# Kernel optimization log

Measured on AMD Instinct MI355X. Metric: run time of the kernel, lower is better.

## Reference

```python
import jax, jax.numpy as jnp
import numpy as np

B, T, D = 2, 2048, 1024
H, HD = 16, 64  # num_heads, key_size

def setup_inputs() -> dict:
    key = jax.random.key(0)
    ks = jax.random.split(key, 5)
    s = 1.0 / np.sqrt(D)  # VarianceScaling(1.0, fan_in) approx
    return {
        "query": jax.random.normal(ks[0], (B, T, D), dtype=jnp.float32),
        "wq": jax.random.normal(ks[1], (D, H * HD), dtype=jnp.float32) * s,
        "bq": jnp.zeros((H * HD,), dtype=jnp.float32),
        "wk": jax.random.normal(ks[2], (D, H * HD), dtype=jnp.float32) * s,
        "bk": jnp.zeros((H * HD,), dtype=jnp.float32),
        "wv": jax.random.normal(ks[3], (D, H * HD), dtype=jnp.float32) * s,
        "bv": jnp.zeros((H * HD,), dtype=jnp.float32),
        "wo": jax.random.normal(ks[4], (H * HD, D), dtype=jnp.float32) * (1.0 / np.sqrt(H * HD)),
        "bo": jnp.zeros((D,), dtype=jnp.float32),
    }

def reference(query, wq, bq, wk, bk, wv, bv, wo, bo):
    b, t, _ = query.shape
    proj = lambda w, bias: (query @ w + bias).reshape(b, t, H, HD)
    q = proj(wq, bq) / np.sqrt(HD).astype(np.float32)  # fixed scaling on queries
    k = proj(wk, bk)
    v = proj(wv, bv)
    logits = jnp.einsum('bthd,bThd->bhtT', q, k)  # [B,H,T,T]
    causal = jnp.tril(jnp.ones((t, t), dtype=logits.dtype))
    logits = logits - 1e10 * (1.0 - causal)
    weights = jax.nn.softmax(logits, axis=-1)
    attn = jnp.einsum('bhtT,bThd->bthd', weights, v)
    attn_vec = attn.reshape(b, t, H * HD)
    return attn_vec @ wo + bo
```

## Files before the change

kernel.cpp:

```cpp
#include <hip/hip_runtime.h>
#include <hip/hip_bf16.h>
#include <stdint.h>
#include <math.h>

typedef short bf16x8 __attribute__((ext_vector_type(8)));
typedef float f32x4 __attribute__((ext_vector_type(4)));
typedef unsigned u32x4v __attribute__((ext_vector_type(4)));
typedef __hip_bfloat16 bf16;

#define MFMA16(a, b, c) __builtin_amdgcn_mfma_f32_16x16x32_bf16((a), (b), (c), 0, 0, 0)

__device__ __forceinline__ void glds16(const void* g, void* l) {
  __builtin_amdgcn_global_load_lds((const __attribute__((address_space(1))) void*)g,
                                   (__attribute__((address_space(3))) void*)l, 16, 0, 0);
}

__device__ __forceinline__ bf16x8 ld8(const bf16* p) {
  return *reinterpret_cast<const bf16x8*>(p);
}

__device__ __forceinline__ void pl32swap(unsigned& a, unsigned& b) {
  asm volatile("v_permlane32_swap_b32 %0, %1" : "+v"(a), "+v"(b));
}
__device__ __forceinline__ void pl16swap(unsigned& a, unsigned& b) {
  asm volatile("v_permlane16_swap_b32 %0, %1" : "+v"(a), "+v"(b));
}


__global__ void k_prep(const float* __restrict__ query,
                       const float* __restrict__ wq, const float* __restrict__ wk,
                       const float* __restrict__ wv, const float* __restrict__ wo,
                       bf16* __restrict__ X, bf16* __restrict__ Wqkvt, bf16* __restrict__ Wot) {
  __shared__ float tile[32][33];
  const int z = blockIdx.z;
  if (z < 4) {
    const float* src = (z == 0) ? wq : (z == 1) ? wk : (z == 2) ? wv : wo;
    bf16* dst = (z < 3) ? (Wqkvt + (size_t)z * 1024 * 1024) : Wot;
    const int tx = threadIdx.x & 31, ty = threadIdx.x >> 5;
    const int x = blockIdx.x * 32 + tx;
    const int y0 = blockIdx.y * 32;
#pragma unroll
    for (int i = 0; i < 4; ++i) tile[ty + i * 8][tx] = src[(size_t)(y0 + ty + i * 8) * 1024 + x];
    __syncthreads();
#pragma unroll
    for (int i = 0; i < 4; ++i) {
      int c = blockIdx.x * 32 + ty + i * 8;
      dst[(size_t)c * 1024 + y0 + tx] = __float2bfloat16(tile[tx][ty + i * 8]);
    }
  } else {
    const int vb = (z - 4) * 1024 + blockIdx.y * 32 + blockIdx.x;
    const int i = vb * 256 + threadIdx.x;
    float4 v = reinterpret_cast<const float4*>(query)[i];
    bf16 a0 = __float2bfloat16(v.x), a1 = __float2bfloat16(v.y);
    bf16 a2 = __float2bfloat16(v.z), a3 = __float2bfloat16(v.w);
    ushort4 r;
    r.x = reinterpret_cast<unsigned short&>(a0);
    r.y = reinterpret_cast<unsigned short&>(a1);
    r.z = reinterpret_cast<unsigned short&>(a2);
    r.w = reinterpret_cast<unsigned short&>(a3);
    reinterpret_cast<ushort4*>(X)[i] = r;
  }
}


__device__ __forceinline__ void gemm_core(const bf16* __restrict__ A, const bf16* __restrict__ Bt,
                                          int K, int arow0, int bcol0,
                                          bf16* As, bf16* Bs, f32x4 acc[4][4]) {
  const int tid = threadIdx.x, lane = tid & 63, w = tid >> 6;
  const int rsub = lane >> 3, slot = lane & 7;
  const int srcslot = slot ^ rsub;
  const int wrow = (w >> 1) * 64, wcol = (w & 1) * 64;
  const int lr = lane & 15, lg = lane >> 4;
  const int nkt = K >> 6;
  for (int kt = 0; kt < nkt; ++kt) {
    const int k0 = kt * 64;
    if (kt) __syncthreads();
#pragma unroll
    for (int i = 0; i < 4; ++i) {
      const int chunk = w * 4 + i;
      glds16(A + (size_t)(arow0 + chunk * 8 + rsub) * K + k0 + srcslot * 8, As + chunk * 512);
      glds16(Bt + (size_t)(bcol0 + chunk * 8 + rsub) * K + k0 + srcslot * 8, Bs + chunk * 512);
    }
    __syncthreads();
#pragma unroll
    for (int kk = 0; kk < 2; ++kk) {
      bf16x8 af[4], bfv[4];
#pragma unroll
      for (int m = 0; m < 4; ++m) {
        const int row = wrow + m * 16 + lr;
        const int byte = (row * 128 + ((kk * 32 + lg * 8) << 1)) ^ ((row & 7) << 4);
        af[m] = *reinterpret_cast<const bf16x8*>(reinterpret_cast<const char*>(As) + byte);
      }
#pragma unroll
      for (int n = 0; n < 4; ++n) {
        const int row = wcol + n * 16 + lr;
        const int byte = (row * 128 + ((kk * 32 + lg * 8) << 1)) ^ ((row & 7) << 4);
        bfv[n] = *reinterpret_cast<const bf16x8*>(reinterpret_cast<const char*>(Bs) + byte);
      }
#pragma unroll
      for (int m = 0; m < 4; ++m)
#pragma unroll
        for (int n = 0; n < 4; ++n) acc[m][n] = MFMA16(af[m], bfv[n], acc[m][n]);
    }
  }
}


__global__ __launch_bounds__(256) void k_gemm_qkv(
    const bf16* __restrict__ X, const bf16* __restrict__ Wt,
    const float* __restrict__ bq, const float* __restrict__ bk, const float* __restrict__ bv,
    bf16* __restrict__ Qo, bf16* __restrict__ Ko, bf16* __restrict__ Vt) {
  __shared__ bf16 As[128 * 64], Bs[128 * 64];
  f32x4 acc[4][4];
#pragma unroll
  for (int i = 0; i < 4; ++i)
#pragma unroll
    for (int j = 0; j < 4; ++j) acc[i][j] = (f32x4){0.f, 0.f, 0.f, 0.f};
  const int arow0 = blockIdx.y * 128, bcol0 = blockIdx.x * 128;
  gemm_core(X, Wt, 1024, arow0, bcol0, As, Bs, acc);
  const int lane = threadIdx.x & 63, w = threadIdx.x >> 6;
  const int wrow = (w >> 1) * 64, wcol = (w & 1) * 64;
  const int lr = lane & 15, lg = lane >> 4;
  const float QSCALE = 0.125f * 1.4426950408889634f;
#pragma unroll
  for (int mi = 0; mi < 4; ++mi) {
#pragma unroll
    for (int ni = 0; ni < 4; ++ni) {
      const int r0 = arow0 + wrow + mi * 16 + lg * 4;
      const int col = bcol0 + wcol + ni * 16 + lr;
      const int which = col >> 10, cw = col & 1023, h = cw >> 6, hd = cw & 63;
      const int b = r0 >> 11, t0 = r0 & 2047;
      if (which == 2) {
        const float bias = bv[cw];
        ushort4 pk;
#pragma unroll
        for (int j = 0; j < 4; ++j) {
          bf16 hv = __float2bfloat16(acc[mi][ni][j] + bias);
          reinterpret_cast<unsigned short*>(&pk)[j] = reinterpret_cast<unsigned short&>(hv);
        }
        *reinterpret_cast<ushort4*>(Vt + ((size_t)((b * 16 + h) * 64 + hd)) * 2048 + t0) = pk;
      } else {
        const float bias = which ? bk[cw] : bq[cw];
        const float scale = which ? 1.0f : QSCALE;
        bf16* dst = which ? Ko : Qo;
#pragma unroll
        for (int j = 0; j < 4; ++j) {
          float v = (acc[mi][ni][j] + bias) * scale;
          dst[((size_t)((b * 16 + h) * 2048) + t0 + j) * 64 + hd] = __float2bfloat16(v);
        }
      }
    }
  }
}


__global__ __launch_bounds__(256) void k_attn(const bf16* __restrict__ Q, const bf16* __restrict__ Kc,
                                              const bf16* __restrict__ Vt, bf16* __restrict__ attn) {
  __shared__ bf16 Ks[2][64 * 64];
  __shared__ bf16 Vs[2][64 * 64];
  const int lane = threadIdx.x & 63, w = threadIdx.x >> 6;
  const int lr = lane & 15, lg = lane >> 4;
  const int rsub = lane >> 3, slot = lane & 7;
  const int srcslot = slot ^ rsub;
  const int bh = blockIdx.x;
  const int qt = 31 - blockIdx.y;
  const int b = bh >> 4, h = bh & 15;
  const bf16* Qp = Q + (size_t)bh * 2048 * 64;
  const bf16* Kp = Kc + (size_t)bh * 2048 * 64;
  const bf16* Vp = Vt + (size_t)bh * 64 * 2048;

  const int q0 = qt * 64 + w * 16;
  const bf16x8 qa0 = ld8(Qp + (size_t)(q0 + lr) * 64 + lg * 8);
  const bf16x8 qa1 = ld8(Qp + (size_t)(q0 + lr) * 64 + 32 + lg * 8);
  f32x4 o[4], ol;
#pragma unroll
  for (int n = 0; n < 4; ++n) o[n] = (f32x4){0.f, 0.f, 0.f, 0.f};
  ol = (f32x4){0.f, 0.f, 0.f, 0.f};
  const int nkv = qt + 1;
  const float MBIAS = -8.0f * 1.4426950408889634f;
  const f32x4 minit = {MBIAS, MBIAS, MBIAS, MBIAS};
  const short one_bf = (short)0x3F80;
  const bf16x8 ones = {one_bf, one_bf, one_bf, one_bf, one_bf, one_bf, one_bf, one_bf};

#pragma unroll
  for (int i = 0; i < 2; ++i) {
    const int ck = w * 2 + i;
    glds16(Kp + (size_t)(ck * 8 + rsub) * 64 + srcslot * 8, &Ks[0][ck * 512]);
    glds16(Vp + (size_t)(ck * 8 + rsub) * 2048 + srcslot * 8, &Vs[0][ck * 512]);
  }
  __syncthreads();
  int cur = 0;

#pragma unroll 1
  for (int it = 0; it < nkv; ++it) {
    if (it + 1 < nkv) {
#pragma unroll
      for (int i = 0; i < 2; ++i) {
        const int ck = w * 2 + i;
        glds16(Kp + (size_t)((it + 1) * 64 + ck * 8 + rsub) * 64 + srcslot * 8, &Ks[cur ^ 1][ck * 512]);
        glds16(Vp + (size_t)(ck * 8 + rsub) * 2048 + (it + 1) * 64 + srcslot * 8, &Vs[cur ^ 1][ck * 512]);
      }
    }
    f32x4 s[4];
    const char* Kb = reinterpret_cast<const char*>(&Ks[cur][0]);
#pragma unroll
    for (int n = 0; n < 4; ++n) {
      const int row = n * 16 + lr;
      const int rsw = (row & 7) << 4;
      bf16x8 kb0 = *reinterpret_cast<const bf16x8*>(Kb + ((row * 128 + lg * 16) ^ rsw));
      bf16x8 kb1 = *reinterpret_cast<const bf16x8*>(Kb + ((row * 128 + 64 + lg * 16) ^ rsw));
      s[n] = MFMA16(kb0, qa0, minit);
      s[n] = MFMA16(kb1, qa1, s[n]);
    }
    if (it == nkv - 1) {
      const int qme = q0 + lr - it * 64 - lg * 4;
#pragma unroll
      for (int n = 0; n < 4; ++n)
#pragma unroll
        for (int j = 0; j < 4; ++j)
          if (n * 16 + j > qme) s[n][j] = -1e30f;
    }
    float p[4][4];
#pragma unroll
    for (int n = 0; n < 4; ++n)
#pragma unroll
      for (int j = 0; j < 4; ++j) p[n][j] = __builtin_amdgcn_exp2f(s[n][j]);
    unsigned pw[4][2];
#pragma unroll
    for (int n = 0; n < 4; ++n) {
      pw[n][0] = __builtin_amdgcn_perm(__float_as_uint(p[n][1]), __float_as_uint(p[n][0]), 0x07060302u);
      pw[n][1] = __builtin_amdgcn_perm(__float_as_uint(p[n][3]), __float_as_uint(p[n][2]), 0x07060302u);
    }
#pragma unroll
    for (int n1 = 0; n1 < 2; ++n1)
#pragma unroll
      for (int hh = 0; hh < 2; ++hh) {
        pl32swap(pw[2 * n1][hh], pw[2 * n1 + 1][hh]);
        pl16swap(pw[2 * n1][hh], pw[2 * n1 + 1][hh]);
      }
    bf16x8 pa[2];
#pragma unroll
    for (int n1 = 0; n1 < 2; ++n1) {
      u32x4v tv = (u32x4v){pw[2 * n1][0], pw[2 * n1][1], pw[2 * n1 + 1][0], pw[2 * n1 + 1][1]};
      pa[n1] = __builtin_bit_cast(bf16x8, tv);
    }
    ol = MFMA16(pa[0], ones, ol);
    ol = MFMA16(pa[1], ones, ol);
    const char* Vb = reinterpret_cast<const char*>(&Vs[cur][0]);
#pragma unroll
    for (int n2 = 0; n2 < 4; ++n2) {
#pragma unroll
      for (int kc = 0; kc < 2; ++kc) {
        const int row = n2 * 16 + lr;
        const int rsw = (row & 7) << 4;
        bf16x8 vb = *reinterpret_cast<const bf16x8*>(Vb + ((row * 128 + (kc * 32 + lg * 8) * 2) ^ rsw));
        o[n2] = MFMA16(pa[kc], vb, o[n2]);
      }
    }
    __syncthreads();
    cur ^= 1;
  }
#pragma unroll
  for (int j = 0; j < 4; ++j) {
    const float inv = 1.0f / ol[j];
    const int qq = q0 + lg * 4 + j;
#pragma unroll
    for (int n2 = 0; n2 < 4; ++n2)
      attn[((size_t)(b * 2048 + qq)) * 1024 + h * 64 + n2 * 16 + lr] = __float2bfloat16(o[n2][j] * inv);
  }
}


__global__ __launch_bounds__(256) void k_gemm_out(const bf16* __restrict__ A, const bf16* __restrict__ Wot,
                                                  const float* __restrict__ bo, float* __restrict__ out) {
  __shared__ bf16 As[64 * 64], Bs[128 * 64];
  f32x4 acc[4][2];
#pragma unroll
  for (int i = 0; i < 4; ++i)
#pragma unroll
    for (int j = 0; j < 2; ++j) acc[i][j] = (f32x4){0.f, 0.f, 0.f, 0.f};
  const int arow0 = blockIdx.y * 64, bcol0 = blockIdx.x * 128;
  const int lane = threadIdx.x & 63, w = threadIdx.x >> 6;
  const int rsub = lane >> 3, slot = lane & 7;
  const int srcslot = slot ^ rsub;
  const int lr = lane & 15, lg = lane >> 4;
  for (int kt = 0; kt < 16; ++kt) {
    const int k0 = kt * 64;
    if (kt) __syncthreads();
#pragma unroll
    for (int i = 0; i < 2; ++i) {
      const int chunk = w * 2 + i;
      glds16(A + (size_t)(arow0 + chunk * 8 + rsub) * 1024 + k0 + srcslot * 8, As + chunk * 512);
    }
#pragma unroll
    for (int i = 0; i < 4; ++i) {
      const int chunk = w * 4 + i;
      glds16(Wot + (size_t)(bcol0 + chunk * 8 + rsub) * 1024 + k0 + srcslot * 8, Bs + chunk * 512);
    }
    __syncthreads();
#pragma unroll
    for (int kk = 0; kk < 2; ++kk) {
      bf16x8 af[4], bfv[2];
#pragma unroll
      for (int m = 0; m < 4; ++m) {
        const int row = m * 16 + lr;
        const int byte = (row * 128 + ((kk * 32 + lg * 8) << 1)) ^ ((row & 7) << 4);
        af[m] = *reinterpret_cast<const bf16x8*>(reinterpret_cast<const char*>(As) + byte);
      }
#pragma unroll
      for (int n = 0; n < 2; ++n) {
        const int row = w * 32 + n * 16 + lr;
        const int byte = (row * 128 + ((kk * 32 + lg * 8) << 1)) ^ ((row & 7) << 4);
        bfv[n] = *reinterpret_cast<const bf16x8*>(reinterpret_cast<const char*>(Bs) + byte);
      }
#pragma unroll
      for (int m = 0; m < 4; ++m)
#pragma unroll
        for (int n = 0; n < 2; ++n) acc[m][n] = MFMA16(af[m], bfv[n], acc[m][n]);
    }
  }
#pragma unroll
  for (int mi = 0; mi < 4; ++mi) {
#pragma unroll
    for (int ni = 0; ni < 2; ++ni) {
      const int r0 = arow0 + mi * 16 + lg * 4;
      const int col = bcol0 + w * 32 + ni * 16 + lr;
      const float bias = bo[col];
#pragma unroll
      for (int j = 0; j < 4; ++j) out[(size_t)(r0 + j) * 1024 + col] = acc[mi][ni][j] + bias;
    }
  }
}


extern "C" void kernel_launch(void* const* d_in, const int* in_sizes, int n_in,
                              void* d_out, int out_size, void* d_ws, size_t ws_size,
                              hipStream_t stream) {
  const float* query = (const float*)d_in[0];
  const float* wq = (const float*)d_in[1];
  const float* bq = (const float*)d_in[2];
  const float* wk = (const float*)d_in[3];
  const float* bk = (const float*)d_in[4];
  const float* wv = (const float*)d_in[5];
  const float* bv = (const float*)d_in[6];
  const float* wo = (const float*)d_in[7];
  const float* bo = (const float*)d_in[8];
  float* out = (float*)d_out;
  char* ws = (char*)d_ws;
  const size_t MB = 1u << 20;
  bf16* X     = (bf16*)(ws + 0);
  bf16* Wqkvt = (bf16*)(ws + 8 * MB);
  bf16* Wot   = (bf16*)(ws + 14 * MB);
  bf16* Qb    = (bf16*)(ws + 16 * MB);
  bf16* Kb    = (bf16*)(ws + 24 * MB);
  bf16* Vt    = (bf16*)(ws + 32 * MB);
  bf16* attn  = (bf16*)(ws + 40 * MB);

  k_prep<<<dim3(32, 32, 8), 256, 0, stream>>>(query, wq, wk, wv, wo, X, Wqkvt, Wot);
  k_gemm_qkv<<<dim3(24, 32), 256, 0, stream>>>(X, Wqkvt, bq, bk, bv, Qb, Kb, Vt);
  k_attn<<<dim3(32, 32), 256, 0, stream>>>(Qb, Kb, Vt, attn);
  k_gemm_out<<<dim3(8, 64), 256, 0, stream>>>(attn, Wot, bo, out);
}
```

Measured before the change: 96.12 us.

## Load K and V fragments directly from global memory in attention kernel

Removes the double-buffered LDS staging of K and V tiles in the attention kernel and has each wave read its MFMA operand fragments straight from global memory (through the caches). This drops the shared-memory footprint and the per-iteration barrier, which can raise occupancy and lets waves run independently. In exchange, the four waves in a block each fetch the same K/V tile, so L1/L2 traffic and load latency grow, and there is no explicit prefetch to hide that latency.

Measured after the change: 203.0 us. 2.11x slower.

```diff
diff --git a/kernel.cpp b/kernel.cpp
--- a/kernel.cpp
+++ b/kernel.cpp
@@ -156,12 +156,8 @@
 
 __global__ __launch_bounds__(256) void k_attn(const bf16* __restrict__ Q, const bf16* __restrict__ Kc,
                                               const bf16* __restrict__ Vt, bf16* __restrict__ attn) {
-  __shared__ bf16 Ks[2][64 * 64];
-  __shared__ bf16 Vs[2][64 * 64];
   const int lane = threadIdx.x & 63, w = threadIdx.x >> 6;
   const int lr = lane & 15, lg = lane >> 4;
-  const int rsub = lane >> 3, slot = lane & 7;
-  const int srcslot = slot ^ rsub;
   const int bh = blockIdx.x;
   const int qt = 31 - blockIdx.y;
   const int b = bh >> 4, h = bh & 15;
@@ -182,38 +178,22 @@
   const short one_bf = (short)0x3F80;
   const bf16x8 ones = {one_bf, one_bf, one_bf, one_bf, one_bf, one_bf, one_bf, one_bf};
 
-#pragma unroll
-  for (int i = 0; i < 2; ++i) {
-    const int ck = w * 2 + i;
-    glds16(Kp + (size_t)(ck * 8 + rsub) * 64 + srcslot * 8, &Ks[0][ck * 512]);
-    glds16(Vp + (size_t)(ck * 8 + rsub) * 2048 + srcslot * 8, &Vs[0][ck * 512]);
-  }
-  __syncthreads();
-  int cur = 0;
+  const bf16* Kl = Kp + (size_t)lr * 64 + lg * 8;
+  const bf16* Vl = Vp + (size_t)lr * 2048 + lg * 8;
 
 #pragma unroll 1
   for (int it = 0; it < nkv; ++it) {
-    if (it + 1 < nkv) {
-#pragma unroll
-      for (int i = 0; i < 2; ++i) {
-        const int ck = w * 2 + i;
-        glds16(Kp + (size_t)((it + 1) * 64 + ck * 8 + rsub) * 64 + srcslot * 8, &Ks[cur ^ 1][ck * 512]);
-        glds16(Vp + (size_t)(ck * 8 + rsub) * 2048 + (it + 1) * 64 + srcslot * 8, &Vs[cur ^ 1][ck * 512]);
-      }
-    }
+    const int kv0 = it * 64;
     f32x4 s[4];
-    const char* Kb = reinterpret_cast<const char*>(&Ks[cur][0]);
 #pragma unroll
     for (int n = 0; n < 4; ++n) {
-      const int row = n * 16 + lr;
-      const int rsw = (row & 7) << 4;
-      bf16x8 kb0 = *reinterpret_cast<const bf16x8*>(Kb + ((row * 128 + lg * 16) ^ rsw));
-      bf16x8 kb1 = *reinterpret_cast<const bf16x8*>(Kb + ((row * 128 + 64 + lg * 16) ^ rsw));
+      bf16x8 kb0 = ld8(Kl + (size_t)(kv0 + n * 16) * 64);
+      bf16x8 kb1 = ld8(Kl + (size_t)(kv0 + n * 16) * 64 + 32);
       s[n] = MFMA16(kb0, qa0, minit);
       s[n] = MFMA16(kb1, qa1, s[n]);
     }
     if (it == nkv - 1) {
-      const int qme = q0 + lr - it * 64 - lg * 4;
+      const int qme = q0 + lr - kv0 - lg * 4;
 #pragma unroll
       for (int n = 0; n < 4; ++n)
 #pragma unroll
@@ -246,19 +226,14 @@
     }
     ol = MFMA16(pa[0], ones, ol);
     ol = MFMA16(pa[1], ones, ol);
-    const char* Vb = reinterpret_cast<const char*>(&Vs[cur][0]);
 #pragma unroll
     for (int n2 = 0; n2 < 4; ++n2) {
 #pragma unroll
       for (int kc = 0; kc < 2; ++kc) {
-        const int row = n2 * 16 + lr;
-        const int rsw = (row & 7) << 4;
-        bf16x8 vb = *reinterpret_cast<const bf16x8*>(Vb + ((row * 128 + (kc * 32 + lg * 8) * 2) ^ rsw));
+        bf16x8 vb = ld8(Vl + (size_t)n2 * 16 * 2048 + kv0 + kc * 32);
         o[n2] = MFMA16(pa[kc], vb, o[n2]);
       }
     }
-    __syncthreads();
-    cur ^= 1;
   }
 #pragma unroll
   for (int j = 0; j < 4; ++j) {
```
